# Kernel optimization log

Hardware: AMD Instinct MI355X
Metric: run time of the kernel (lower is better)

Reference implementation:

```python
import jax, jax.numpy as jnp
import numpy as np

N_NODES = 50000
N_EDGES = 600000
EMB = 128

def setup_inputs() -> dict:
    key = jax.random.key(0)
    ks = jax.random.split(key, 6)
    h = jax.random.normal(ks[0], (N_NODES, EMB), dtype=jnp.float32)
    edge_attr = jax.random.normal(ks[1], (N_EDGES, EMB), dtype=jnp.float32)
    src = jax.random.randint(ks[2], (N_EDGES,), 0, N_NODES, dtype=jnp.int32)
    dst = jax.random.randint(ks[3], (N_EDGES,), 0, N_NODES, dtype=jnp.int32)
    # MLP: Linear(emb, 2*emb) -> ReLU -> Linear(2*emb, emb)
    W1 = jax.random.normal(ks[4], (EMB, 2 * EMB), dtype=jnp.float32) * (1.0 / np.sqrt(EMB))
    b1 = jnp.zeros((2 * EMB,), dtype=jnp.float32)
    W2 = jax.random.normal(ks[5], (2 * EMB, EMB), dtype=jnp.float32) * (1.0 / np.sqrt(2 * EMB))
    b2 = jnp.zeros((EMB,), dtype=jnp.float32)
    eps = jnp.zeros((1,), dtype=jnp.float32)
    return {"h": h, "edge_attr": edge_attr, "src": src, "dst": dst,
            "W1": W1, "b1": b1, "W2": W2, "b2": b2, "eps": eps}

def reference(h, edge_attr, src, dst, W1, b1, W2, b2, eps):
    # message: m_e = h[src_e] + edge_attr_e   (edge_encoder is None)
    m = h[src] + edge_attr                              # [E, D]
    # reduce: sum messages per destination node
    aggr = jax.ops.segment_sum(m, dst, num_segments=N_NODES)  # [N, D]
    # out = (1 + eps) * h + MLP(aggr)
    hidden = jax.nn.relu(aggr @ W1 + b1)                # [N, 2D]
    mlp_out = hidden @ W2 + b2                          # [N, D]
    return (1.0 + eps) * h + mlp_out
```

## Files before the change

kernel.cpp:

```cpp
#include <hip/hip_runtime.h>

#define N_NODES 50000
#define N_EDGES 600000
#define D 128
#define H2 256
#define TN 16
#define MAXC 2048

typedef float f4 __attribute__((ext_vector_type(4)));
typedef unsigned int u4 __attribute__((ext_vector_type(4)));

__device__ __forceinline__ f4 ldg_nt(const float* p) {
    return __builtin_nontemporal_load((const f4*)p);
}
__device__ __forceinline__ f4 ldg(const float* p) {
    return *(const f4*)p;
}

__device__ __forceinline__ unsigned int bfpair(float lo, float hi) {
    unsigned int ul = __float_as_uint(lo), uh = __float_as_uint(hi);
    ul += 0x7FFFu + ((ul >> 16) & 1u);
    uh += 0x7FFFu + ((uh >> 16) & 1u);
    return (ul >> 16) | (uh & 0xFFFF0000u);
}
__device__ __forceinline__ float bflo(unsigned int u) { return __uint_as_float(u << 16); }
__device__ __forceinline__ float bfhi(unsigned int u) { return __uint_as_float(u & 0xFFFF0000u); }

__global__ __launch_bounds__(256) void hcvt_kernel(const float* __restrict__ h,
                                                   u4* __restrict__ hb4) {
    const int i = blockIdx.x * 256 + threadIdx.x;
    if (i < (N_NODES * D) / 8) {
        const f4 v0 = ldg(h + (size_t)i * 8);
        const f4 v1 = ldg(h + (size_t)i * 8 + 4);
        u4 o;
        o.x = bfpair(v0[0], v0[1]);
        o.y = bfpair(v0[2], v0[3]);
        o.z = bfpair(v1[0], v1[1]);
        o.w = bfpair(v1[2], v1[3]);
        hb4[i] = o;
    }
}

__global__ __launch_bounds__(256) void hist_kernel(const int* __restrict__ dst,
                                                   int* __restrict__ counts) {
    unsigned int e = blockIdx.x * 256u + threadIdx.x;
    if (e < N_EDGES) atomicAdd(&counts[dst[e]], 1);
}

__global__ __launch_bounds__(256) void scan1_kernel(const int* __restrict__ counts,
                                                    int* __restrict__ scanned,
                                                    int* __restrict__ blocksums) {
    __shared__ int wsum[4];
    const int tid = threadIdx.x;
    const int lane = tid & 63;
    const int wv = tid >> 6;
    const int i = blockIdx.x * 256 + tid;
    const int cval = (i < N_NODES) ? counts[i] : 0;
    int x = cval;
    #pragma unroll
    for (int d = 1; d < 64; d <<= 1) {
        int t = __shfl_up(x, d, 64);
        if (lane >= d) x += t;
    }
    if (lane == 63) wsum[wv] = x;
    __syncthreads();
    if (tid == 0) {
        int s = 0;
        #pragma unroll
        for (int w = 0; w < 4; ++w) { s += wsum[w]; wsum[w] = s; }
    }
    __syncthreads();
    const int prefix = (wv > 0 ? wsum[wv - 1] : 0) + (x - cval);
    if (i < N_NODES) scanned[i] = prefix;
    if (tid == 0) blocksums[blockIdx.x] = wsum[3];
}

__global__ __launch_bounds__(256) void scan2_kernel(const int* __restrict__ blocksums,
                                                    int* __restrict__ blockbase, int nb) {
    __shared__ int wsum[4];
    const int tid = threadIdx.x;
    const int lane = tid & 63;
    const int wv = tid >> 6;
    const int cval = (tid < nb) ? blocksums[tid] : 0;
    int x = cval;
    #pragma unroll
    for (int d = 1; d < 64; d <<= 1) {
        int t = __shfl_up(x, d, 64);
        if (lane >= d) x += t;
    }
    if (lane == 63) wsum[wv] = x;
    __syncthreads();
    if (tid == 0) {
        int s = 0;
        #pragma unroll
        for (int w = 0; w < 4; ++w) { s += wsum[w]; wsum[w] = s; }
    }
    __syncthreads();
    if (tid < nb) blockbase[tid] = (wv > 0 ? wsum[wv - 1] : 0) + (x - cval);
}

__global__ __launch_bounds__(256) void scan3_kernel(const int* __restrict__ scanned,
                                                    const int* __restrict__ blockbase,
                                                    int* __restrict__ offsets,
                                                    int* __restrict__ cursor) {
    const int i = blockIdx.x * 256 + threadIdx.x;
    if (i < N_NODES) {
        const int v = scanned[i] + blockbase[blockIdx.x];
        offsets[i] = v;
        cursor[i] = v;
    }
    if (i == 0) offsets[N_NODES] = N_EDGES;
}

__global__ __launch_bounds__(256) void scatter_kernel(const int* __restrict__ src,
                                                      const int* __restrict__ dst,
                                                      int* __restrict__ cursor,
                                                      int2* __restrict__ perm2) {
    unsigned int e = blockIdx.x * 256u + threadIdx.x;
    if (e >= N_EDGES) return;
    const int d = dst[e];
    const int p = atomicAdd(&cursor[d], 1);
    perm2[p] = make_int2((int)(e * D), src[e] * D);
}

__global__ __launch_bounds__(256, 6) void fused_kernel(
    const float* __restrict__ h, const float* __restrict__ ea,
    const unsigned int* __restrict__ hb,
    const int* __restrict__ offsets, const int2* __restrict__ perm2,
    const float* __restrict__ W1, const float* __restrict__ b1,
    const float* __restrict__ W2, const float* __restrict__ b2,
    const float* __restrict__ eps, float* __restrict__ out)
{
    __shared__ float s_lds[5120];
    int2* s_perm = (int2*)s_lds;
    unsigned int* s_aggr = (unsigned int*)s_lds;
    float* s_w = s_lds + 1024;
    unsigned int* s_hid = (unsigned int*)(s_lds + 3072);

    const int tid = threadIdx.x;
    const int t  = tid >> 4;
    const int c8 = (tid & 15) << 3;
    const int node0 = blockIdx.x * TN;
    const int blkbeg = offsets[node0];
    const int blkend = offsets[node0 + TN];
    const int nbeg = offsets[node0 + t];
    const int nend = offsets[node0 + t + 1];

    f4 a0 = (f4)(0.f);
    f4 a1 = (f4)(0.f);

    for (int cb = blkbeg; cb < blkend; cb += MAXC) {
        const int cnt = min(blkend - cb, MAXC);
        __syncthreads();
        for (int i = tid; i < cnt; i += 256) s_perm[i] = perm2[cb + i];
        __syncthreads();
        const int lo = max(nbeg - cb, 0);
        const int hi = min(nend - cb, cnt);
        int j = lo;
        for (; j + 3 < hi; j += 4) {
            int2 p[4];
            #pragma unroll
            for (int q = 0; q < 4; ++q) p[q] = s_perm[j + q];
            f4 ev0[4], ev1[4];
            u4 hu[4];
            #pragma unroll
            for (int q = 0; q < 4; ++q) {
                const float* er = ea + (size_t)(unsigned)p[q].x + c8;
                ev0[q] = ldg_nt(er);
                ev1[q] = ldg_nt(er + 4);
                hu[q]  = *(const u4*)(hb + (((unsigned)p[q].y + c8) >> 1));
            }
            #pragma unroll
            for (int q = 0; q < 4; ++q) {
                f4 hv0, hv1;
                hv0[0] = bflo(hu[q].x); hv0[1] = bfhi(hu[q].x);
                hv0[2] = bflo(hu[q].y); hv0[3] = bfhi(hu[q].y);
                hv1[0] = bflo(hu[q].z); hv1[1] = bfhi(hu[q].z);
                hv1[2] = bflo(hu[q].w); hv1[3] = bfhi(hu[q].w);
                a0 += ev0[q] + hv0;
                a1 += ev1[q] + hv1;
            }
        }
        for (; j < hi; ++j) {
            const int2 p = s_perm[j];
            const float* er = ea + (size_t)(unsigned)p.x + c8;
            const f4 e0 = ldg_nt(er);
            const f4 e1 = ldg_nt(er + 4);
            const u4 u = *(const u4*)(hb + (((unsigned)p.y + c8) >> 1));
            f4 hv0, hv1;
            hv0[0] = bflo(u.x); hv0[1] = bfhi(u.x);
            hv0[2] = bflo(u.y); hv0[3] = bfhi(u.y);
            hv1[0] = bflo(u.z); hv1[1] = bfhi(u.z);
            hv1[2] = bflo(u.w); hv1[3] = bfhi(u.w);
            a0 += e0 + hv0;
            a1 += e1 + hv1;
        }
    }
    __syncthreads();
    {
        unsigned int* ad = s_aggr + t * 64 + (c8 >> 1);
        ad[0] = bfpair(a0[0], a0[1]);
        ad[1] = bfpair(a0[2], a0[3]);
        ad[2] = bfpair(a1[0], a1[1]);
        ad[3] = bfpair(a1[2], a1[3]);
    }

    const int j0 = (tid & 63) << 2;
    const int tbase = (tid >> 6) << 2;
    {
        float4 acc1[4];
        const float4 bv = *(const float4*)(b1 + j0);
        #pragma unroll
        for (int q = 0; q < 4; ++q) acc1[q] = bv;
        for (int k0 = 0; k0 < D; k0 += 8) {
            __syncthreads();
            {
                const float4* srcw = (const float4*)(W1 + (size_t)k0 * H2);
                float4* dstl = (float4*)s_w;
                dstl[tid]       = srcw[tid];
                dstl[tid + 256] = srcw[tid + 256];
            }
            __syncthreads();
            #pragma unroll
            for (int kk = 0; kk < 8; kk += 4) {
                float4 w[4];
                #pragma unroll
                for (int q = 0; q < 4; ++q)
                    w[q] = *(const float4*)&s_w[(kk + q) * H2 + j0];
                #pragma unroll
                for (int u = 0; u < 4; ++u) {
                    const unsigned int* ar = s_aggr + (tbase + u) * 64 + ((k0 + kk) >> 1);
                    const unsigned int u01 = ar[0];
                    const unsigned int u23 = ar[1];
                    float4 a;
                    a.x = bflo(u01); a.y = bfhi(u01);
                    a.z = bflo(u23); a.w = bfhi(u23);
                    acc1[u].x = fmaf(a.x, w[0].x, acc1[u].x);
                    acc1[u].y = fmaf(a.x, w[0].y, acc1[u].y);
                    acc1[u].z = fmaf(a.x, w[0].z, acc1[u].z);
                    acc1[u].w = fmaf(a.x, w[0].w, acc1[u].w);
                    acc1[u].x = fmaf(a.y, w[1].x, acc1[u].x);
                    acc1[u].y = fmaf(a.y, w[1].y, acc1[u].y);
                    acc1[u].z = fmaf(a.y, w[1].z, acc1[u].z);
                    acc1[u].w = fmaf(a.y, w[1].w, acc1[u].w);
                    acc1[u].x = fmaf(a.z, w[2].x, acc1[u].x);
                    acc1[u].y = fmaf(a.z, w[2].y, acc1[u].y);
                    acc1[u].z = fmaf(a.z, w[2].z, acc1[u].z);
                    acc1[u].w = fmaf(a.z, w[2].w, acc1[u].w);
                    acc1[u].x = fmaf(a.w, w[3].x, acc1[u].x);
                    acc1[u].y = fmaf(a.w, w[3].y, acc1[u].y);
                    acc1[u].z = fmaf(a.w, w[3].z, acc1[u].z);
                    acc1[u].w = fmaf(a.w, w[3].w, acc1[u].w);
                }
            }
        }
        #pragma unroll
        for (int u = 0; u < 4; ++u) {
            unsigned int* hd = s_hid + (tbase + u) * 128 + (j0 >> 1);
            hd[0] = bfpair(fmaxf(acc1[u].x, 0.f), fmaxf(acc1[u].y, 0.f));
            hd[1] = bfpair(fmaxf(acc1[u].z, 0.f), fmaxf(acc1[u].w, 0.f));
        }
    }

    {
        const int i0 = (tid & 31) << 2;
        const int g = tid >> 5;
        float4 acc2[2];
        const float4 bv = *(const float4*)(b2 + i0);
        acc2[0] = bv; acc2[1] = bv;
        for (int k0 = 0; k0 < H2; k0 += 16) {
            __syncthreads();
            {
                const float4* srcw = (const float4*)(W2 + (size_t)k0 * D);
                float4* dstl = (float4*)s_w;
                dstl[tid]       = srcw[tid];
                dstl[tid + 256] = srcw[tid + 256];
            }
            __syncthreads();
            #pragma unroll
            for (int kk = 0; kk < 16; kk += 4) {
                float4 w[4];
                #pragma unroll
                for (int q = 0; q < 4; ++q)
                    w[q] = *(const float4*)&s_w[(kk + q) * D + i0];
                #pragma unroll
                for (int u = 0; u < 2; ++u) {
                    const unsigned int* hr = s_hid + (g + u * 8) * 128 + ((k0 + kk) >> 1);
                    const unsigned int u01 = hr[0];
                    const unsigned int u23 = hr[1];
                    float4 a;
                    a.x = bflo(u01); a.y = bfhi(u01);
                    a.z = bflo(u23); a.w = bfhi(u23);
                    acc2[u].x = fmaf(a.x, w[0].x, acc2[u].x);
                    acc2[u].y = fmaf(a.x, w[0].y, acc2[u].y);
                    acc2[u].z = fmaf(a.x, w[0].z, acc2[u].z);
                    acc2[u].w = fmaf(a.x, w[0].w, acc2[u].w);
                    acc2[u].x = fmaf(a.y, w[1].x, acc2[u].x);
                    acc2[u].y = fmaf(a.y, w[1].y, acc2[u].y);
                    acc2[u].z = fmaf(a.y, w[1].z, acc2[u].z);
                    acc2[u].w = fmaf(a.y, w[1].w, acc2[u].w);
                    acc2[u].x = fmaf(a.z, w[2].x, acc2[u].x);
                    acc2[u].y = fmaf(a.z, w[2].y, acc2[u].y);
                    acc2[u].z = fmaf(a.z, w[2].z, acc2[u].z);
                    acc2[u].w = fmaf(a.z, w[2].w, acc2[u].w);
                    acc2[u].x = fmaf(a.w, w[3].x, acc2[u].x);
                    acc2[u].y = fmaf(a.w, w[3].y, acc2[u].y);
                    acc2[u].z = fmaf(a.w, w[3].z, acc2[u].z);
                    acc2[u].w = fmaf(a.w, w[3].w, acc2[u].w);
                }
            }
        }
        const float ep = 1.0f + eps[0];
        #pragma unroll
        for (int u = 0; u < 2; ++u) {
            const int node = node0 + g + u * 8;
            const f4 hv = ldg(h + (size_t)node * D + i0);
            f4 o;
            o[0] = fmaf(ep, hv[0], acc2[u].x);
            o[1] = fmaf(ep, hv[1], acc2[u].y);
            o[2] = fmaf(ep, hv[2], acc2[u].z);
            o[3] = fmaf(ep, hv[3], acc2[u].w);
            __builtin_nontemporal_store(o, (f4*)(out + (size_t)node * D + i0));
        }
    }
}

extern "C" void kernel_launch(void* const* d_in, const int* in_sizes, int n_in,
                              void* d_out, int out_size, void* d_ws, size_t ws_size,
                              hipStream_t stream) {
    const float* h   = (const float*)d_in[0];
    const float* ea  = (const float*)d_in[1];
    const int*   src = (const int*)d_in[2];
    const int*   dst = (const int*)d_in[3];
    const float* W1  = (const float*)d_in[4];
    const float* b1  = (const float*)d_in[5];
    const float* W2  = (const float*)d_in[6];
    const float* b2  = (const float*)d_in[7];
    const float* eps = (const float*)d_in[8];
    float* out = (float*)d_out;

    char* ws = (char*)d_ws;
    int*  counts    = (int*)ws;
    int*  scanned   = (int*)(ws + 256 * 1024);
    int*  offsets   = (int*)(ws + 512 * 1024);
    int*  cursor    = (int*)(ws + 768 * 1024);
    int*  blocksums = (int*)(ws + 1008 * 1024);
    int*  blockbase = (int*)(ws + 1012 * 1024);
    int2* perm2     = (int2*)(ws + 1024 * 1024);
    unsigned int* hbm = (unsigned int*)(ws + 6 * 1024 * 1024);

    hipMemsetAsync(counts, 0, N_NODES * sizeof(int), stream);

    const int eblocks = (N_EDGES + 255) / 256;
    const int nblocks = (N_NODES + 255) / 256;

    hcvt_kernel<<<(N_NODES * D / 8 + 255) / 256, 256, 0, stream>>>(h, (u4*)hbm);
    hist_kernel<<<eblocks, 256, 0, stream>>>(dst, counts);
    scan1_kernel<<<nblocks, 256, 0, stream>>>(counts, scanned, blocksums);
    scan2_kernel<<<1, 256, 0, stream>>>(blocksums, blockbase, nblocks);
    scan3_kernel<<<nblocks, 256, 0, stream>>>(scanned, blockbase, offsets, cursor);
    scatter_kernel<<<eblocks, 256, 0, stream>>>(src, dst, cursor, perm2);
    fused_kernel<<<N_NODES / TN, 256, 0, stream>>>(
        h, ea, hbm, offsets, perm2, W1, b1, W2, b2, eps, out);
}
```

Before: 583.1 us.

## Compute fused MLP with bf16 MFMA using pre-transposed bf16 weights

Replaces the scalar FMA MLP stage in the fused kernel with MFMA 16x16x32 bf16 instructions. A new small kernel converts W1 and W2 to bf16 in a transposed layout so B fragments load straight from global memory, which removes the per-tile LDS weight staging and its barriers. Aggregates and hidden activations are stored in LDS with an XOR swizzle to avoid bank conflicts, and the output passes through LDS to reach a coalesced layout. This cuts the ALU cost of the per-block MLP. In exchange it adds weight fragment reads from global or L2 per block and relies on bf16 precision for the weights.

```diff
diff --git a/kernel.cpp b/kernel.cpp
--- a/kernel.cpp
+++ b/kernel.cpp
@@ -9,6 +9,7 @@
 
 typedef float f4 __attribute__((ext_vector_type(4)));
 typedef unsigned int u4 __attribute__((ext_vector_type(4)));
+typedef short s8v __attribute__((ext_vector_type(8)));
 
 __device__ __forceinline__ f4 ldg_nt(const float* p) {
     return __builtin_nontemporal_load((const f4*)p);
@@ -22,6 +23,11 @@
     ul += 0x7FFFu + ((ul >> 16) & 1u);
     uh += 0x7FFFu + ((uh >> 16) & 1u);
     return (ul >> 16) | (uh & 0xFFFF0000u);
+}
+__device__ __forceinline__ unsigned short bf16of(float v) {
+    unsigned int u = __float_as_uint(v);
+    u += 0x7FFFu + ((u >> 16) & 1u);
+    return (unsigned short)(u >> 16);
 }
 __device__ __forceinline__ float bflo(unsigned int u) { return __uint_as_float(u << 16); }
 __device__ __forceinline__ float bfhi(unsigned int u) { return __uint_as_float(u & 0xFFFF0000u); }
@@ -38,6 +44,21 @@
         o.z = bfpair(v1[0], v1[1]);
         o.w = bfpair(v1[2], v1[3]);
         hb4[i] = o;
+    }
+}
+
+__global__ __launch_bounds__(256) void wcvt_kernel(const float* __restrict__ W1,
+                                                   const float* __restrict__ W2,
+                                                   unsigned int* __restrict__ w1t,
+                                                   unsigned int* __restrict__ w2t) {
+    const int tid = blockIdx.x * 256 + threadIdx.x;
+    if (tid < 256 * 64) {
+        const int n = tid >> 6, kp = tid & 63;
+        w1t[tid] = bfpair(W1[(size_t)(2 * kp) * H2 + n], W1[(size_t)(2 * kp + 1) * H2 + n]);
+    } else if (tid < 256 * 64 + 128 * 128) {
+        const int t2 = tid - 256 * 64;
+        const int n = t2 >> 7, kp = t2 & 127;
+        w2t[t2] = bfpair(W2[(size_t)(2 * kp) * D + n], W2[(size_t)(2 * kp + 1) * D + n]);
     }
 }
 
@@ -126,16 +147,17 @@
 __global__ __launch_bounds__(256, 6) void fused_kernel(
     const float* __restrict__ h, const float* __restrict__ ea,
     const unsigned int* __restrict__ hb,
+    const unsigned short* __restrict__ w1t, const unsigned short* __restrict__ w2t,
     const int* __restrict__ offsets, const int2* __restrict__ perm2,
-    const float* __restrict__ W1, const float* __restrict__ b1,
-    const float* __restrict__ W2, const float* __restrict__ b2,
+    const float* __restrict__ b1, const float* __restrict__ b2,
     const float* __restrict__ eps, float* __restrict__ out)
 {
     __shared__ float s_lds[5120];
     int2* s_perm = (int2*)s_lds;
-    unsigned int* s_aggr = (unsigned int*)s_lds;
-    float* s_w = s_lds + 1024;
-    unsigned int* s_hid = (unsigned int*)(s_lds + 3072);
+    unsigned int* s_aggrU = (unsigned int*)s_lds;
+    unsigned int* s_hidU  = (unsigned int*)(s_lds + 1024);
+    unsigned short* s_hid16 = (unsigned short*)(s_lds + 1024);
+    float* s_outF = s_lds + 3072;
 
     const int tid = threadIdx.x;
     const int t  = tid >> 4;
@@ -198,128 +220,85 @@
     }
     __syncthreads();
     {
-        unsigned int* ad = s_aggr + t * 64 + (c8 >> 1);
-        ad[0] = bfpair(a0[0], a0[1]);
-        ad[1] = bfpair(a0[2], a0[3]);
-        ad[2] = bfpair(a1[0], a1[1]);
-        ad[3] = bfpair(a1[2], a1[3]);
-    }
-
-    const int j0 = (tid & 63) << 2;
-    const int tbase = (tid >> 6) << 2;
+        u4 av;
+        av.x = bfpair(a0[0], a0[1]);
+        av.y = bfpair(a0[2], a0[3]);
+        av.z = bfpair(a1[0], a1[1]);
+        av.w = bfpair(a1[2], a1[3]);
+        const int ai = (t * 64 + ((tid & 15) << 2)) ^ ((t & 7) << 2);
+        *(u4*)(s_aggrU + ai) = av;
+    }
+    __syncthreads();
+
+    const int lane = tid & 63;
+    const int wid = tid >> 6;
+    const int r = lane & 15;
+    const int g = lane >> 4;
+
     {
-        float4 acc1[4];
-        const float4 bv = *(const float4*)(b1 + j0);
-        #pragma unroll
-        for (int q = 0; q < 4; ++q) acc1[q] = bv;
-        for (int k0 = 0; k0 < D; k0 += 8) {
-            __syncthreads();
-            {
-                const float4* srcw = (const float4*)(W1 + (size_t)k0 * H2);
-                float4* dstl = (float4*)s_w;
-                dstl[tid]       = srcw[tid];
-                dstl[tid + 256] = srcw[tid + 256];
-            }
-            __syncthreads();
-            #pragma unroll
-            for (int kk = 0; kk < 8; kk += 4) {
-                float4 w[4];
-                #pragma unroll
-                for (int q = 0; q < 4; ++q)
-                    w[q] = *(const float4*)&s_w[(kk + q) * H2 + j0];
-                #pragma unroll
-                for (int u = 0; u < 4; ++u) {
-                    const unsigned int* ar = s_aggr + (tbase + u) * 64 + ((k0 + kk) >> 1);
-                    const unsigned int u01 = ar[0];
-                    const unsigned int u23 = ar[1];
-                    float4 a;
-                    a.x = bflo(u01); a.y = bfhi(u01);
-                    a.z = bflo(u23); a.w = bfhi(u23);
-                    acc1[u].x = fmaf(a.x, w[0].x, acc1[u].x);
-                    acc1[u].y = fmaf(a.x, w[0].y, acc1[u].y);
-                    acc1[u].z = fmaf(a.x, w[0].z, acc1[u].z);
-                    acc1[u].w = fmaf(a.x, w[0].w, acc1[u].w);
-                    acc1[u].x = fmaf(a.y, w[1].x, acc1[u].x);
-                    acc1[u].y = fmaf(a.y, w[1].y, acc1[u].y);
-                    acc1[u].z = fmaf(a.y, w[1].z, acc1[u].z);
-                    acc1[u].w = fmaf(a.y, w[1].w, acc1[u].w);
-                    acc1[u].x = fmaf(a.z, w[2].x, acc1[u].x);
-                    acc1[u].y = fmaf(a.z, w[2].y, acc1[u].y);
-                    acc1[u].z = fmaf(a.z, w[2].z, acc1[u].z);
-                    acc1[u].w = fmaf(a.z, w[2].w, acc1[u].w);
-                    acc1[u].x = fmaf(a.w, w[3].x, acc1[u].x);
-                    acc1[u].y = fmaf(a.w, w[3].y, acc1[u].y);
-                    acc1[u].z = fmaf(a.w, w[3].z, acc1[u].z);
-                    acc1[u].w = fmaf(a.w, w[3].w, acc1[u].w);
-                }
-            }
-        }
-        #pragma unroll
-        for (int u = 0; u < 4; ++u) {
-            unsigned int* hd = s_hid + (tbase + u) * 128 + (j0 >> 1);
-            hd[0] = bfpair(fmaxf(acc1[u].x, 0.f), fmaxf(acc1[u].y, 0.f));
-            hd[1] = bfpair(fmaxf(acc1[u].z, 0.f), fmaxf(acc1[u].w, 0.f));
-        }
-    }
+        s8v afr[4];
+        #pragma unroll
+        for (int ks = 0; ks < 4; ++ks)
+            afr[ks] = *(const s8v*)(s_aggrU + ((r * 64 + ks * 16 + g * 4) ^ ((r & 7) << 2)));
+        #pragma unroll
+        for (int i = 0; i < 4; ++i) {
+            const int n0 = (wid * 4 + i) * 16;
+            f4 acc = (f4)(0.f);
+            #pragma unroll
+            for (int ks = 0; ks < 4; ++ks) {
+                const s8v bfr = *(const s8v*)(w1t + (size_t)(n0 + r) * 128 + ks * 32 + g * 8);
+                acc = __builtin_amdgcn_mfma_f32_16x16x32_bf16(afr[ks], bfr, acc, 0, 0, 0);
+            }
+            const int c = n0 + r;
+            const float b1c = b1[c];
+            #pragma unroll
+            for (int reg = 0; reg < 4; ++reg) {
+                const int rd = g * 4 + reg;
+                const float v = fmaxf(acc[reg] + b1c, 0.f);
+                const int ui = (rd * 128 + (c >> 1)) ^ ((rd & 7) << 2);
+                s_hid16[ui * 2 + (c & 1)] = bf16of(v);
+            }
+        }
+    }
+    __syncthreads();
+
+    {
+        s8v hfr[8];
+        #pragma unroll
+        for (int ks = 0; ks < 8; ++ks)
+            hfr[ks] = *(const s8v*)(s_hidU + ((r * 128 + ks * 16 + g * 4) ^ ((r & 7) << 2)));
+        #pragma unroll
+        for (int i = 0; i < 2; ++i) {
+            const int n0 = (wid * 2 + i) * 16;
+            f4 acc = (f4)(0.f);
+            #pragma unroll
+            for (int ks = 0; ks < 8; ++ks) {
+                const s8v bfr = *(const s8v*)(w2t + (size_t)(n0 + r) * 256 + ks * 32 + g * 8);
+                acc = __builtin_amdgcn_mfma_f32_16x16x32_bf16(hfr[ks], bfr, acc, 0, 0, 0);
+            }
+            #pragma unroll
+            for (int reg = 0; reg < 4; ++reg)
+                s_outF[(g * 4 + reg) * 128 + n0 + r] = acc[reg];
+        }
+    }
+    __syncthreads();
 
     {
         const int i0 = (tid & 31) << 2;
-        const int g = tid >> 5;
-        float4 acc2[2];
-        const float4 bv = *(const float4*)(b2 + i0);
-        acc2[0] = bv; acc2[1] = bv;
-        for (int k0 = 0; k0 < H2; k0 += 16) {
-            __syncthreads();
-            {
-                const float4* srcw = (const float4*)(W2 + (size_t)k0 * D);
-                float4* dstl = (float4*)s_w;
-                dstl[tid]       = srcw[tid];
-                dstl[tid + 256] = srcw[tid + 256];
-            }
-            __syncthreads();
-            #pragma unroll
-            for (int kk = 0; kk < 16; kk += 4) {
-                float4 w[4];
-                #pragma unroll
-                for (int q = 0; q < 4; ++q)
-                    w[q] = *(const float4*)&s_w[(kk + q) * D + i0];
-                #pragma unroll
-                for (int u = 0; u < 2; ++u) {
-                    const unsigned int* hr = s_hid + (g + u * 8) * 128 + ((k0 + kk) >> 1);
-                    const unsigned int u01 = hr[0];
-                    const unsigned int u23 = hr[1];
-                    float4 a;
-                    a.x = bflo(u01); a.y = bfhi(u01);
-                    a.z = bflo(u23); a.w = bfhi(u23);
-                    acc2[u].x = fmaf(a.x, w[0].x, acc2[u].x);
-                    acc2[u].y = fmaf(a.x, w[0].y, acc2[u].y);
-                    acc2[u].z = fmaf(a.x, w[0].z, acc2[u].z);
-                    acc2[u].w = fmaf(a.x, w[0].w, acc2[u].w);
-                    acc2[u].x = fmaf(a.y, w[1].x, acc2[u].x);
-                    acc2[u].y = fmaf(a.y, w[1].y, acc2[u].y);
-                    acc2[u].z = fmaf(a.y, w[1].z, acc2[u].z);
-                    acc2[u].w = fmaf(a.y, w[1].w, acc2[u].w);
-                    acc2[u].x = fmaf(a.z, w[2].x, acc2[u].x);
-                    acc2[u].y = fmaf(a.z, w[2].y, acc2[u].y);
-                    acc2[u].z = fmaf(a.z, w[2].z, acc2[u].z);
-                    acc2[u].w = fmaf(a.z, w[2].w, acc2[u].w);
-                    acc2[u].x = fmaf(a.w, w[3].x, acc2[u].x);
-                    acc2[u].y = fmaf(a.w, w[3].y, acc2[u].y);
-                    acc2[u].z = fmaf(a.w, w[3].z, acc2[u].z);
-                    acc2[u].w = fmaf(a.w, w[3].w, acc2[u].w);
-                }
-            }
-        }
+        const int gg = tid >> 5;
         const float ep = 1.0f + eps[0];
+        const f4 b2v = ldg(b2 + i0);
         #pragma unroll
         for (int u = 0; u < 2; ++u) {
-            const int node = node0 + g + u * 8;
+            const int nl = gg + u * 8;
+            const int node = node0 + nl;
+            const f4 sv = *(const f4*)&s_outF[nl * 128 + i0];
             const f4 hv = ldg(h + (size_t)node * D + i0);
             f4 o;
-            o[0] = fmaf(ep, hv[0], acc2[u].x);
-            o[1] = fmaf(ep, hv[1], acc2[u].y);
-            o[2] = fmaf(ep, hv[2], acc2[u].z);
-            o[3] = fmaf(ep, hv[3], acc2[u].w);
+            o[0] = sv[0] + b2v[0] + ep * hv[0];
+            o[1] = sv[1] + b2v[1] + ep * hv[1];
+            o[2] = sv[2] + b2v[2] + ep * hv[2];
+            o[3] = sv[3] + b2v[3] + ep * hv[3];
             __builtin_nontemporal_store(o, (f4*)(out + (size_t)node * D + i0));
         }
     }
@@ -348,6 +327,8 @@
     int*  blockbase = (int*)(ws + 1012 * 1024);
     int2* perm2     = (int2*)(ws + 1024 * 1024);
     unsigned int* hbm = (unsigned int*)(ws + 6 * 1024 * 1024);
+    unsigned int* w1t = (unsigned int*)(ws + 20 * 1024 * 1024);
+    unsigned int* w2t = (unsigned int*)(ws + 21 * 1024 * 1024);
 
     hipMemsetAsync(counts, 0, N_NODES * sizeof(int), stream);
 
@@ -355,11 +336,13 @@
     const int nblocks = (N_NODES + 255) / 256;
 
     hcvt_kernel<<<(N_NODES * D / 8 + 255) / 256, 256, 0, stream>>>(h, (u4*)hbm);
+    wcvt_kernel<<<128, 256, 0, stream>>>(W1, W2, w1t, w2t);
     hist_kernel<<<eblocks, 256, 0, stream>>>(dst, counts);
     scan1_kernel<<<nblocks, 256, 0, stream>>>(counts, scanned, blocksums);
     scan2_kernel<<<1, 256, 0, stream>>>(blocksums, blockbase, nblocks);
     scan3_kernel<<<nblocks, 256, 0, stream>>>(scanned, blockbase, offsets, cursor);
     scatter_kernel<<<eblocks, 256, 0, stream>>>(src, dst, cursor, perm2);
     fused_kernel<<<N_NODES / TN, 256, 0, stream>>>(
-        h, ea, hbm, offsets, perm2, W1, b1, W2, b2, eps, out);
-}
+        h, ea, hbm, (const unsigned short*)w1t, (const unsigned short*)w2t,
+        offsets, perm2, b1, b2, eps, out);
+}
```

New measurement: 549.6 us. -5.7%, faster.
